# Kernel optimization log

Hardware: AMD Instinct MI355X
Metric: run time of the kernel (lower is better)

Reference implementation:

```python
import jax, jax.numpy as jnp
import numpy as np

B = 4096      # batch
D = 64        # state_dim
H = 512       # hidden_dim


def setup_inputs() -> dict:
    key = jax.random.key(0)
    ks = jax.random.split(key, 16)

    def init(k, shape, fan_in):
        return jax.random.normal(k, shape, dtype=jnp.float32) / np.float32(np.sqrt(fan_in))

    mu = jax.random.normal(ks[0], (B, D), dtype=jnp.float32)
    sigma_diag = 0.1 * jax.random.uniform(ks[1], (B, D), dtype=jnp.float32) + 0.01
    states = jnp.concatenate([mu, sigma_diag], axis=1)  # [B, 2D]

    return {
        "t": jnp.float32(0.5),
        "states": states,
        # dynamics net: tanh MLP D -> H -> H -> D
        "W1": init(ks[2], (H, D), D), "b1": jnp.zeros((H,), jnp.float32),
        "W2": init(ks[3], (H, H), H), "b2": jnp.zeros((H,), jnp.float32),
        "W3": init(ks[4], (D, H), H), "b3": jnp.zeros((D,), jnp.float32),
        # process-noise net: tanh MLP D -> H -> H -> D, softplus head (diagonal Q)
        "V1": init(ks[5], (H, D), D), "c1": jnp.zeros((H,), jnp.float32),
        "V2": init(ks[6], (H, H), H), "c2": jnp.zeros((H,), jnp.float32),
        "V3": init(ks[7], (D, H), H), "c3": jnp.zeros((D,), jnp.float32),
    }


def reference(t, states, W1, b1, W2, b2, W3, b3, V1, c1, V2, c2, V3, c3):
    # UPN ODE function, diagonal-covariance path.
    mu = states[:, :D]          # [B, D]
    sigma_diag = states[:, D:]  # [B, D]

    # dynamics MLP forward (t is an autonomous-system placeholder, unused)
    h1 = jnp.tanh(mu @ W1.T + b1)   # [B, H]
    h2 = jnp.tanh(h1 @ W2.T + b2)   # [B, H]
    mu_drift = h2 @ W3.T + b3       # [B, D]

    # analytic batched Jacobian of the tanh MLP: J = W3 diag(1-h2^2) W2 diag(1-h1^2) W1
    d1 = 1.0 - h1 * h1              # [B, H]
    d2 = 1.0 - h2 * h2              # [B, H]
    inner = jnp.einsum('hk,bk,kd->bhd', W2, d1, W1)   # [B, H, D]
    J = jnp.einsum('oh,bh,bhd->bod', W3, d2, inner)   # [B, D, D]
    J_diag = jnp.diagonal(J, axis1=1, axis2=2)        # [B, D]

    # process-noise net: diagonal Q, softplus ensures positivity
    g1 = jnp.tanh(mu @ V1.T + c1)
    g2 = jnp.tanh(g1 @ V2.T + c2)
    Q_diag = jax.nn.softplus(g2 @ V3.T + c3)          # [B, D]

    sigma_drift = 2.0 * J_diag * sigma_diag + Q_diag  # [B, D]
    return jnp.concatenate([mu_drift, sigma_drift], axis=1)  # [B, 2D]
```

## Files before the change

### kernel.cpp

```cpp
#include <hip/hip_runtime.h>
#include <hip/hip_bf16.h>

#define BB 4096
#define DD 64
#define HH 512

typedef __hip_bfloat16 bf16;
typedef _Float16 f16;
typedef __attribute__((ext_vector_type(8))) short bf16x8;
typedef __attribute__((ext_vector_type(8))) _Float16 f16x8;
typedef __attribute__((ext_vector_type(4))) float f32x4;

__device__ __forceinline__ float bf2f(bf16 x) { return __bfloat162float(x); }
__device__ __forceinline__ float u16tof(unsigned short u) {
  union { unsigned int i; float f; } v; v.i = ((unsigned int)u) << 16; return v.f;
}
#define BC8(p) __builtin_bit_cast(bf16x8, *(const uint4*)(p))
#define BCH8(p) __builtin_bit_cast(f16x8, *(const uint4*)(p))

__device__ __forceinline__ void gl16(const void* g, void* l) {
  __builtin_amdgcn_global_load_lds((__attribute__((address_space(1))) void*)g,
                                   (__attribute__((address_space(3))) void*)l,
                                   16, 0, 0);
}

#define BARRIER() __builtin_amdgcn_s_barrier()
#define LGKM0() do { asm volatile("s_waitcnt lgkmcnt(0)" ::: "memory"); \
                     __builtin_amdgcn_sched_barrier(0); } while (0)


__global__ __launch_bounds__(256) void cvt_weights(
    const float* __restrict__ W2, const float* __restrict__ V2,
    const float* __restrict__ W1, const float* __restrict__ V1,
    const float* __restrict__ W3, const float* __restrict__ V3,
    bf16* __restrict__ W2bf, bf16* __restrict__ V2bf,
    bf16* __restrict__ W1bf, bf16* __restrict__ V1bf,
    bf16* __restrict__ W3bf, bf16* __restrict__ V3bf,
    f16* __restrict__ W2sw, f16* __restrict__ W1sw, float* __restrict__ W3T) {
  int blk = blockIdx.x, t = threadIdx.x;
  if (blk < 512) {
    const float* src = (blk < 256) ? W2 : V2;
    bf16* dst = (blk < 256) ? W2bf : V2bf;
    int i = ((blk & 255) * 256 + t) * 4;
    float4 v = *(const float4*)(src + i);
    bf16 o[4] = {__float2bfloat16(v.x), __float2bfloat16(v.y),
                 __float2bfloat16(v.z), __float2bfloat16(v.w)};
    *(uint2*)(dst + i) = *(uint2*)o;
  } else if (blk < 640) {
    int uid = (blk - 512) * 256 + t;
    int kc = uid >> 12, rem = uid & 4095;
    int h = rem >> 3, u = rem & 7;
    const float* src = W2 + (size_t)h * HH + kc * 64 + u * 8;
    float4 a = *(const float4*)src;
    float4 b = *(const float4*)(src + 4);
    f16 o[8] = {(f16)a.x, (f16)a.y, (f16)a.z, (f16)a.w,
                (f16)b.x, (f16)b.y, (f16)b.z, (f16)b.w};
    *(uint4*)(W2sw + (size_t)((kc * 512 + h) * 8 + (u ^ (h & 7))) * 8) = *(uint4*)o;
  } else if (blk < 656) {
    int uid = (blk - 640) * 256 + t;
    int kc = uid >> 9, rem = uid & 511;
    int dl = rem >> 3, u = rem & 7;
    f16 o[8];
#pragma unroll
    for (int e = 0; e < 8; ++e)
      o[e] = (f16)W1[(size_t)(kc * 64 + u * 8 + e) * DD + dl];
    *(uint4*)(W1sw + (size_t)((kc * 64 + dl) * 8 + (u ^ (dl & 7))) * 8) = *(uint4*)o;
  } else if (blk < 784) {
    int which = (blk - 656) >> 5;
    int local = (blk - 656) & 31;
    const float* src = (which == 0) ? W1 : (which == 1) ? V1 : (which == 2) ? W3 : V3;
    bf16* dst = (which == 0) ? W1bf : (which == 1) ? V1bf : (which == 2) ? W3bf : V3bf;
    int i = (local * 256 + t) * 4;
    float4 v = *(const float4*)(src + i);
    bf16 o[4] = {__float2bfloat16(v.x), __float2bfloat16(v.y),
                 __float2bfloat16(v.z), __float2bfloat16(v.w)};
    *(uint2*)(dst + i) = *(uint2*)o;
  } else {
    int e = ((blk - 784) * 256 + t) * 4;
    int h = e >> 6, o0 = e & 63;
    float o[4];
#pragma unroll
    for (int j = 0; j < 4; ++j) o[j] = W3[(size_t)(o0 + j) * HH + h];
    *(float4*)(W3T + (size_t)h * 64 + o0) = *(float4*)o;
  }
}

__global__ __launch_bounds__(256) void fwd(
    const float* __restrict__ states,
    const bf16* __restrict__ W1bf, const float* __restrict__ b1,
    const bf16* __restrict__ W2bf, const float* __restrict__ b2,
    const bf16* __restrict__ W3bf, const float* __restrict__ b3,
    const bf16* __restrict__ V1bf, const float* __restrict__ c1,
    const bf16* __restrict__ V2bf, const float* __restrict__ c2,
    const bf16* __restrict__ V3bf, const float* __restrict__ c3,
    bf16* __restrict__ Xbf, bf16* __restrict__ Ybf, float* __restrict__ out) {
  __shared__ __align__(16) bf16 mus[16 * 72];
  __shared__ __align__(16) bf16 Xres[16 * 520];
  __shared__ __align__(16) bf16 Bs[128 * 72];
  __shared__ __align__(16) bf16 Ych[16 * 136];
  const int bt = blockIdx.x * 16;
  const int path = blockIdx.y;
  const bf16* Wa = path ? V1bf : W1bf;
  const float* ba = path ? c1 : b1;
  const bf16* Wb = path ? V2bf : W2bf;
  const float* bbv = path ? c2 : b2;
  const bf16* Wc = path ? V3bf : W3bf;
  const float* bcv = path ? c3 : b3;
  const int t = threadIdx.x;
  const int lane = t & 63;
  const int w = t >> 6;
  const int c = lane & 15, q = lane >> 4;

  if (t < 128) {
    int row = t >> 3, cg = (t & 7) * 8;
    bf16 o[8];
#pragma unroll
    for (int j = 0; j < 8; j += 4) {
      float4 v = *(const float4*)(states + (size_t)(bt + row) * 128 + cg + j);
      o[j] = __float2bfloat16(v.x); o[j + 1] = __float2bfloat16(v.y);
      o[j + 2] = __float2bfloat16(v.z); o[j + 3] = __float2bfloat16(v.w);
    }
    *(uint4*)(mus + row * 72 + cg) = *(const uint4*)o;
  }
  __syncthreads();

  for (int nch = 0; nch < 4; ++nch) {
    if (nch) __syncthreads();
#pragma unroll
    for (int i = 0; i < 4; ++i) {
      int g = t + i * 256;
      int row = g >> 3, kb = (g & 7) * 8;
      *(uint4*)(Bs + row * 72 + kb) =
          *(const uint4*)(Wa + (size_t)(nch * 128 + row) * 64 + kb);
    }
    __syncthreads();
    f32x4 acc1[2] = {};
#pragma unroll
    for (int s = 0; s < 2; ++s) {
      bf16x8 af = BC8(mus + c * 72 + s * 32 + q * 8);
#pragma unroll
      for (int nt = 0; nt < 2; ++nt) {
        bf16x8 bfr = BC8(Bs + (w * 32 + nt * 16 + c) * 72 + s * 32 + q * 8);
        acc1[nt] = __builtin_amdgcn_mfma_f32_16x16x32_bf16(af, bfr, acc1[nt], 0, 0, 0);
      }
    }
#pragma unroll
    for (int nt = 0; nt < 2; ++nt) {
      int col = nch * 128 + w * 32 + nt * 16 + c;
      float bias = ba[col];
#pragma unroll
      for (int r = 0; r < 4; ++r) {
        int row = q * 4 + r;
        float x = tanhf(acc1[nt][r] + bias);
        Xres[row * 520 + col] = __float2bfloat16(x);
        if (!path) Xbf[(size_t)(bt + row) * HH + col] = __float2bfloat16(x);
      }
    }
  }
  __syncthreads();

  f32x4 acc3 = {};
  for (int hch = 0; hch < 4; ++hch) {
    f32x4 acc2[2] = {};
    for (int kc = 0; kc < 8; ++kc) {
      __syncthreads();
#pragma unroll
      for (int i = 0; i < 4; ++i) {
        int g = t + i * 256;
        int row = g >> 3, kb = (g & 7) * 8;
        *(uint4*)(Bs + row * 72 + kb) =
            *(const uint4*)(Wb + (size_t)(hch * 128 + row) * HH + kc * 64 + kb);
      }
      __syncthreads();
#pragma unroll
      for (int s = 0; s < 2; ++s) {
        bf16x8 af = BC8(Xres + c * 520 + kc * 64 + s * 32 + q * 8);
#pragma unroll
        for (int nt = 0; nt < 2; ++nt) {
          bf16x8 bfr = BC8(Bs + (w * 32 + nt * 16 + c) * 72 + s * 32 + q * 8);
          acc2[nt] = __builtin_amdgcn_mfma_f32_16x16x32_bf16(af, bfr, acc2[nt], 0, 0, 0);
        }
      }
    }
    __syncthreads();
#pragma unroll
    for (int nt = 0; nt < 2; ++nt) {
      int hl = w * 32 + nt * 16 + c;
      int h = hch * 128 + hl;
      float bias = bbv[h];
#pragma unroll
      for (int r = 0; r < 4; ++r) {
        int row = q * 4 + r;
        float y = tanhf(acc2[nt][r] + bias);
        Ych[row * 136 + hl] = __float2bfloat16(y);
        if (!path) Ybf[(size_t)(bt + row) * HH + h] = __float2bfloat16(y);
      }
    }
    __syncthreads();
#pragma unroll
    for (int s3 = 0; s3 < 4; ++s3) {
      bf16x8 bf3 = BC8(Wc + (size_t)(w * 16 + c) * HH + hch * 128 + s3 * 32 + q * 8);
      bf16x8 af3 = BC8(Ych + c * 136 + s3 * 32 + q * 8);
      acc3 = __builtin_amdgcn_mfma_f32_16x16x32_bf16(af3, bf3, acc3, 0, 0, 0);
    }
  }
  {
    int o = w * 16 + c;
    float bias = bcv[o];
#pragma unroll
    for (int r = 0; r < 4; ++r) {
      int row = q * 4 + r;
      float v = acc3[r] + bias;
      if (path) {
        v = fmaxf(v, 0.0f) + log1pf(expf(-fabsf(v)));
        out[(size_t)(bt + row) * 128 + 64 + o] = v;
      } else {
        out[(size_t)(bt + row) * 128 + o] = v;
      }
    }
  }
}

#define LDSB(buf) ((buf) * 32768)
#define LDSA(buf) (98304 + (buf) * 8192)
#define LDSD1 122880
#define LDSD2 126976
#define LDSRED 98304

#define STAGE(kc_, buf_) do {                                                  \
    const char* gb_ = (const char*)W2sw + ((size_t)(kc_) * 512 + h0) * 128;    \
    char* lb_ = (char*)lds + LDSB(buf_);                                       \
    gl16(gb_ + t * 16, lb_ + t * 16);                                          \
    gl16(gb_ + 8192 + t * 16, lb_ + 8192 + t * 16);                            \
    gl16(gb_ + 16384 + t * 16, lb_ + 16384 + t * 16);                          \
    gl16(gb_ + 24576 + t * 16, lb_ + 24576 + t * 16);                          \
    gl16((const char*)W1sw + (kc_) * 8192 + t * 16,                            \
         (char*)lds + LDSA(buf_) + t * 16);                                    \
  } while (0)

__global__ __launch_bounds__(512, 2) void k4_gemm(
    const bf16* __restrict__ Xbf, const bf16* __restrict__ Ybf,
    const f16* __restrict__ W1sw, const f16* __restrict__ W2sw,
    const float* __restrict__ W3T, float* __restrict__ Jpart) {
  __shared__ __align__(16) char lds[131072];
  const int bt = blockIdx.x;
  const int h0 = blockIdx.y * 256;
  const int t = threadIdx.x;
  const int lane = t & 63;
  const int w = t >> 6;
  const int c = lane & 15, q = lane >> 4;
  const int wr = w >> 2, wc = w & 3;
  const int b0 = bt * 4;

  {
    int e = t * 4, j = e >> 9, k = e & 511;
    ushort4 xv = *(const ushort4*)((const unsigned short*)Xbf +
                                   (size_t)(b0 + j) * HH + k);
    f16 o[4];
    float x;
    x = u16tof(xv.x); o[0] = (f16)(1.f - x * x);
    x = u16tof(xv.y); o[1] = (f16)(1.f - x * x);
    x = u16tof(xv.z); o[2] = (f16)(1.f - x * x);
    x = u16tof(xv.w); o[3] = (f16)(1.f - x * x);
    *(uint2*)(lds + LDSD1 + e * 2) = *(uint2*)o;
  }
  {
    int e = t * 2, j = e >> 8, n = e & 255;
    ushort2 yv = *(const ushort2*)((const unsigned short*)Ybf +
                                   (size_t)(b0 + j) * HH + h0 + n);
    float y0 = u16tof(yv.x), y1 = u16tof(yv.y);
    float2 d2v = {1.f - y0 * y0, 1.f - y1 * y1};
    *(float2*)(lds + LDSD2 + e * 4) = d2v;
  }
  __syncthreads();

  STAGE(0, 0);
  STAGE(1, 1);
  asm volatile("s_waitcnt vmcnt(5)" ::: "memory");
  BARRIER();

  const int cj = c & 7;
  const int j16_0 = ((0 + q) ^ cj) * 16;
  const int j16_1 = ((4 + q) ^ cj) * 16;
  const int arow = c * 128;
  const int brow = (wc * 64 + c) * 128;
  const char* d1b = (const char*)lds + LDSD1 + wr * 2048 + q * 16;

  f32x4 acc[8][4] = {};

#pragma unroll
  for (int kc = 0; kc < 8; ++kc) {
    const char* Bb = (const char*)lds + LDSB(kc % 3);
    const char* Ab = (const char*)lds + LDSA(kc % 3);
    const char* gB2 = (const char*)W2sw + ((size_t)(kc + 2) * 512 + h0) * 128;
    const char* gA2 = (const char*)W1sw + (size_t)(kc + 2) * 8192;
    char* lB2 = (char*)lds + LDSB((kc + 2) % 3);
    char* lA2 = (char*)lds + LDSA((kc + 2) % 3);
    f16x8 av;

    f16x8 b0[4], a0[4];
    f16x8 d00 = BCH8(d1b + kc * 128);
#pragma unroll
    for (int nt = 0; nt < 4; ++nt) b0[nt] = BCH8(Bb + brow + nt * 2048 + j16_0);
#pragma unroll
    for (int i = 0; i < 4; ++i) a0[i] = BCH8(Ab + arow + i * 2048 + j16_0);
    if (kc < 6) {
      gl16(gB2 + t * 16, lB2 + t * 16);
      gl16(gB2 + 8192 + t * 16, lB2 + 8192 + t * 16);
    }
    BARRIER(); LGKM0();
    __builtin_amdgcn_s_setprio(1);
#pragma unroll
    for (int mt = 0; mt < 4; ++mt) {
      av = a0[mt] * d00;
#pragma unroll
      for (int nt = 0; nt < 4; ++nt)
        acc[mt][nt] = __builtin_amdgcn_mfma_f32_16x16x32_f16(
            av, b0[nt], acc[mt][nt], 0, 0, 0);
    }
    __builtin_amdgcn_s_setprio(0);
    BARRIER();

    f16x8 d10 = BCH8(d1b + 1024 + kc * 128);
    if (kc < 6) {
      gl16(gB2 + 16384 + t * 16, lB2 + 16384 + t * 16);
      gl16(gB2 + 24576 + t * 16, lB2 + 24576 + t * 16);
    }
    BARRIER(); LGKM0();
    __builtin_amdgcn_s_setprio(1);
#pragma unroll
    for (int mt = 0; mt < 4; ++mt) {
      av = a0[mt] * d10;
#pragma unroll
      for (int nt = 0; nt < 4; ++nt)
        acc[mt + 4][nt] = __builtin_amdgcn_mfma_f32_16x16x32_f16(
            av, b0[nt], acc[mt + 4][nt], 0, 0, 0);
    }
    __builtin_amdgcn_s_setprio(0);
    BARRIER();

    f16x8 b1[4], a1[4];
    f16x8 d01 = BCH8(d1b + 64 + kc * 128);
#pragma unroll
    for (int nt = 0; nt < 4; ++nt) b1[nt] = BCH8(Bb + brow + nt * 2048 + j16_1);
#pragma unroll
    for (int i = 0; i < 4; ++i) a1[i] = BCH8(Ab + arow + i * 2048 + j16_1);
    if (kc < 6) gl16(gA2 + t * 16, lA2 + t * 16);
    BARRIER(); LGKM0();
    __builtin_amdgcn_s_setprio(1);
#pragma unroll
    for (int mt = 0; mt < 4; ++mt) {
      av = a1[mt] * d01;
#pragma unroll
      for (int nt = 0; nt < 4; ++nt)
        acc[mt][nt] = __builtin_amdgcn_mfma_f32_16x16x32_f16(
            av, b1[nt], acc[mt][nt], 0, 0, 0);
    }
    __builtin_amdgcn_s_setprio(0);
    BARRIER();

    f16x8 d11 = BCH8(d1b + 1024 + 64 + kc * 128);
    BARRIER(); LGKM0();
    __builtin_amdgcn_s_setprio(1);
#pragma unroll
    for (int mt = 0; mt < 4; ++mt) {
      av = a1[mt] * d11;
#pragma unroll
      for (int nt = 0; nt < 4; ++nt)
        acc[mt + 4][nt] = __builtin_amdgcn_mfma_f32_16x16x32_f16(
            av, b1[nt], acc[mt + 4][nt], 0, 0, 0);
    }
    __builtin_amdgcn_s_setprio(0);
    if (kc < 6) {
      asm volatile("s_waitcnt vmcnt(5)" ::: "memory");
      BARRIER();
    } else if (kc == 6) {
      asm volatile("s_waitcnt vmcnt(0)" ::: "memory");
      BARRIER();
    }
  }
  __syncthreads();

#pragma unroll
  for (int i = 0; i < 8; ++i) {
    int e = (t + i * 512) * 4;
    int col = e >> 6, dl0 = e & 63;
    float4 v = *(const float4*)(W3T + (size_t)(h0 + col) * 64 + dl0);
    *(float4*)(lds + (col * 72 + dl0) * 4) = v;
  }
  __syncthreads();

  float d2r[2][4];
#pragma unroll
  for (int bh = 0; bh < 2; ++bh)
#pragma unroll
    for (int nt = 0; nt < 4; ++nt)
      d2r[bh][nt] = *(const float*)(
          lds + LDSD2 + ((wr * 2 + bh) * 256 + wc * 64 + nt * 16 + c) * 4);

  float vsum[8][4] = {};
#pragma unroll
  for (int mt4 = 0; mt4 < 4; ++mt4)
#pragma unroll
    for (int nt = 0; nt < 4; ++nt) {
      f32x4 w3v = *(const f32x4*)(
          lds + ((wc * 64 + nt * 16 + c) * 72 + mt4 * 16 + q * 4) * 4);
#pragma unroll
      for (int bh = 0; bh < 2; ++bh) {
        const int mt = bh * 4 + mt4;
        float sc = d2r[bh][nt];
#pragma unroll
        for (int r = 0; r < 4; ++r)
          vsum[mt][r] += acc[mt][nt][r] * w3v[r] * sc;
      }
    }

#pragma unroll
  for (int mt = 0; mt < 8; ++mt)
#pragma unroll
    for (int r = 0; r < 4; ++r) {
      float v = vsum[mt][r];
      v += __shfl_xor(v, 1);
      v += __shfl_xor(v, 2);
      v += __shfl_xor(v, 4);
      v += __shfl_xor(v, 8);
      if (c == 0)
        *(float*)(lds + LDSRED +
                  (wc * 256 + wr * 128 + mt * 16 + q * 4 + r) * 4) = v;
    }
  __syncthreads();
  if (t < 256) {
    float J = *(const float*)(lds + LDSRED + t * 4) +
              *(const float*)(lds + LDSRED + (256 + t) * 4) +
              *(const float*)(lds + LDSRED + (512 + t) * 4) +
              *(const float*)(lds + LDSRED + (768 + t) * 4);
    Jpart[(size_t)blockIdx.y * (BB * 64) + (size_t)bt * 256 + t] = J;
  }
}

__global__ __launch_bounds__(256) void combine(
    const float* __restrict__ Jpart, const float* __restrict__ states,
    float* __restrict__ out) {
  int idx = blockIdx.x * 256 + threadIdx.x;
  int b = idx >> 6, d = idx & 63;
  const int plane = BB * 64;
  float J = Jpart[idx] + Jpart[plane + idx];
  float sig = states[(size_t)b * 128 + 64 + d];
  float qd = out[(size_t)b * 128 + 64 + d];
  out[(size_t)b * 128 + 64 + d] = 2.0f * J * sig + qd;
}

extern "C" void kernel_launch(void* const* d_in, const int* in_sizes, int n_in,
                              void* d_out, int out_size, void* d_ws, size_t ws_size,
                              hipStream_t stream) {
  const float* states = (const float*)d_in[1];
  const float* W1 = (const float*)d_in[2];
  const float* b1 = (const float*)d_in[3];
  const float* W2 = (const float*)d_in[4];
  const float* b2 = (const float*)d_in[5];
  const float* W3 = (const float*)d_in[6];
  const float* b3 = (const float*)d_in[7];
  const float* V1 = (const float*)d_in[8];
  const float* c1 = (const float*)d_in[9];
  const float* V2 = (const float*)d_in[10];
  const float* c2 = (const float*)d_in[11];
  const float* V3 = (const float*)d_in[12];
  const float* c3 = (const float*)d_in[13];
  float* out = (float*)d_out;

  bf16* Xbf = (bf16*)d_ws;
  bf16* Ybf = Xbf + (size_t)BB * HH;
  bf16* W2bf = Ybf + (size_t)BB * HH;
  bf16* V2bf = W2bf + (size_t)HH * HH;
  bf16* W1bf = V2bf + (size_t)HH * HH;
  bf16* V1bf = W1bf + (size_t)HH * DD;
  bf16* W3bf = V1bf + (size_t)HH * DD;
  bf16* V3bf = W3bf + (size_t)DD * HH;
  f16* W1sw = (f16*)(V3bf + (size_t)DD * HH);
  f16* W2sw = W1sw + (size_t)DD * HH;
  float* W3T = (float*)(W2sw + (size_t)HH * HH);
  float* Jpart = W3T + (size_t)HH * DD;

  cvt_weights<<<dim3(816), 256, 0, stream>>>(W2, V2, W1, V1, W3, V3,
                                             W2bf, V2bf, W1bf, V1bf,
                                             W3bf, V3bf, W2sw, W1sw, W3T);
  fwd<<<dim3(256, 2), 256, 0, stream>>>(states, W1bf, b1, W2bf, b2, W3bf, b3,
                                        V1bf, c1, V2bf, c2, V3bf, c3,
                                        Xbf, Ybf, out);
  k4_gemm<<<dim3(1024, 2), 512, 0, stream>>>(Xbf, Ybf, W1sw, W2sw, W3T, Jpart);
  combine<<<dim3(1024), 256, 0, stream>>>(Jpart, states, out);
}
```

Measured before the change: 281.7 us.

## Software-pipeline LDS fragment loads ahead of MFMA clusters in Jacobian GEMM loop

Restructures the inner K loop so the A/B fragment and d1 loads for the next sub-step come from LDS while the current MFMA cluster runs, replacing the load-then-wait-lgkmcnt(0) pattern. It removes the explicit lgkmcnt waits and sched_barriers, cuts the barriers per iteration from eight to four, and moves the vmcnt wait to mid-iteration. The change adds register pressure from double-buffered fragments and relies on the compiler inserting correct LDS waits around the inline-asm barriers, which could risk races on the triple-buffered LDS.

```diff
diff --git a/kernel.cpp b/kernel.cpp
--- a/kernel.cpp
+++ b/kernel.cpp
@@ -24,9 +24,7 @@
                                    16, 0, 0);
 }
 
-#define BARRIER() __builtin_amdgcn_s_barrier()
-#define LGKM0() do { asm volatile("s_waitcnt lgkmcnt(0)" ::: "memory"); \
-                     __builtin_amdgcn_sched_barrier(0); } while (0)
+#define BARX() asm volatile("s_barrier" ::: "memory")
 
 
 __global__ __launch_bounds__(256) void cvt_weights(
@@ -277,7 +275,7 @@
   STAGE(0, 0);
   STAGE(1, 1);
   asm volatile("s_waitcnt vmcnt(5)" ::: "memory");
-  BARRIER();
+  BARX();
 
   const int cj = c & 7;
   const int j16_0 = ((0 + q) ^ cj) * 16;
@@ -286,98 +284,101 @@
   const int brow = (wc * 64 + c) * 128;
   const char* d1b = (const char*)lds + LDSD1 + wr * 2048 + q * 16;
 
+  f16x8 aS0[4], bS0[4], aS1[4], bS1[4], d00, d10, d01, d11, av;
+#pragma unroll
+  for (int i = 0; i < 4; ++i) aS0[i] = BCH8(lds + LDSA(0) + arow + i * 2048 + j16_0);
+#pragma unroll
+  for (int nt = 0; nt < 4; ++nt) bS0[nt] = BCH8(lds + LDSB(0) + brow + nt * 2048 + j16_0);
+  d00 = BCH8(d1b + 0 * 128);
+  d10 = BCH8(d1b + 1024 + 0 * 128);
+
   f32x4 acc[8][4] = {};
 
 #pragma unroll
   for (int kc = 0; kc < 8; ++kc) {
     const char* Bb = (const char*)lds + LDSB(kc % 3);
     const char* Ab = (const char*)lds + LDSA(kc % 3);
+    const char* Bn = (const char*)lds + LDSB((kc + 1) % 3);
+    const char* An = (const char*)lds + LDSA((kc + 1) % 3);
     const char* gB2 = (const char*)W2sw + ((size_t)(kc + 2) * 512 + h0) * 128;
     const char* gA2 = (const char*)W1sw + (size_t)(kc + 2) * 8192;
     char* lB2 = (char*)lds + LDSB((kc + 2) % 3);
     char* lA2 = (char*)lds + LDSA((kc + 2) % 3);
-    f16x8 av;
-
-    f16x8 b0[4], a0[4];
-    f16x8 d00 = BCH8(d1b + kc * 128);
-#pragma unroll
-    for (int nt = 0; nt < 4; ++nt) b0[nt] = BCH8(Bb + brow + nt * 2048 + j16_0);
-#pragma unroll
-    for (int i = 0; i < 4; ++i) a0[i] = BCH8(Ab + arow + i * 2048 + j16_0);
+
+#pragma unroll
+    for (int i = 0; i < 4; ++i) aS1[i] = BCH8(Ab + arow + i * 2048 + j16_1);
+    d01 = BCH8(d1b + 64 + kc * 128);
     if (kc < 6) {
       gl16(gB2 + t * 16, lB2 + t * 16);
       gl16(gB2 + 8192 + t * 16, lB2 + 8192 + t * 16);
     }
-    BARRIER(); LGKM0();
     __builtin_amdgcn_s_setprio(1);
 #pragma unroll
     for (int mt = 0; mt < 4; ++mt) {
-      av = a0[mt] * d00;
+      av = aS0[mt] * d00;
 #pragma unroll
       for (int nt = 0; nt < 4; ++nt)
         acc[mt][nt] = __builtin_amdgcn_mfma_f32_16x16x32_f16(
-            av, b0[nt], acc[mt][nt], 0, 0, 0);
+            av, bS0[nt], acc[mt][nt], 0, 0, 0);
     }
     __builtin_amdgcn_s_setprio(0);
-    BARRIER();
-
-    f16x8 d10 = BCH8(d1b + 1024 + kc * 128);
+    BARX();
+
+#pragma unroll
+    for (int nt = 0; nt < 4; ++nt) bS1[nt] = BCH8(Bb + brow + nt * 2048 + j16_1);
+    d11 = BCH8(d1b + 1024 + 64 + kc * 128);
     if (kc < 6) {
       gl16(gB2 + 16384 + t * 16, lB2 + 16384 + t * 16);
       gl16(gB2 + 24576 + t * 16, lB2 + 24576 + t * 16);
     }
-    BARRIER(); LGKM0();
     __builtin_amdgcn_s_setprio(1);
 #pragma unroll
     for (int mt = 0; mt < 4; ++mt) {
-      av = a0[mt] * d10;
+      av = aS0[mt] * d10;
 #pragma unroll
       for (int nt = 0; nt < 4; ++nt)
         acc[mt + 4][nt] = __builtin_amdgcn_mfma_f32_16x16x32_f16(
-            av, b0[nt], acc[mt + 4][nt], 0, 0, 0);
+            av, bS0[nt], acc[mt + 4][nt], 0, 0, 0);
     }
     __builtin_amdgcn_s_setprio(0);
-    BARRIER();
-
-    f16x8 b1[4], a1[4];
-    f16x8 d01 = BCH8(d1b + 64 + kc * 128);
-#pragma unroll
-    for (int nt = 0; nt < 4; ++nt) b1[nt] = BCH8(Bb + brow + nt * 2048 + j16_1);
-#pragma unroll
-    for (int i = 0; i < 4; ++i) a1[i] = BCH8(Ab + arow + i * 2048 + j16_1);
+    if (kc < 6)      asm volatile("s_waitcnt vmcnt(4)" ::: "memory");
+    else if (kc == 6) asm volatile("s_waitcnt vmcnt(0)" ::: "memory");
+    BARX();
+
+    if (kc < 7) {
+#pragma unroll
+      for (int i = 0; i < 4; ++i) aS0[i] = BCH8(An + arow + i * 2048 + j16_0);
+      d00 = BCH8(d1b + (kc + 1) * 128);
+    }
     if (kc < 6) gl16(gA2 + t * 16, lA2 + t * 16);
-    BARRIER(); LGKM0();
     __builtin_amdgcn_s_setprio(1);
 #pragma unroll
     for (int mt = 0; mt < 4; ++mt) {
-      av = a1[mt] * d01;
+      av = aS1[mt] * d01;
 #pragma unroll
       for (int nt = 0; nt < 4; ++nt)
         acc[mt][nt] = __builtin_amdgcn_mfma_f32_16x16x32_f16(
-            av, b1[nt], acc[mt][nt], 0, 0, 0);
+            av, bS1[nt], acc[mt][nt], 0, 0, 0);
     }
     __builtin_amdgcn_s_setprio(0);
-    BARRIER();
-
-    f16x8 d11 = BCH8(d1b + 1024 + 64 + kc * 128);
-    BARRIER(); LGKM0();
+    BARX();
+
+    if (kc < 7) {
+#pragma unroll
+      for (int nt = 0; nt < 4; ++nt) bS0[nt] = BCH8(Bn + brow + nt * 2048 + j16_0);
+      d10 = BCH8(d1b + 1024 + (kc + 1) * 128);
+    }
     __builtin_amdgcn_s_setprio(1);
 #pragma unroll
     for (int mt = 0; mt < 4; ++mt) {
-      av = a1[mt] * d11;
+      av = aS1[mt] * d11;
 #pragma unroll
       for (int nt = 0; nt < 4; ++nt)
         acc[mt + 4][nt] = __builtin_amdgcn_mfma_f32_16x16x32_f16(
-            av, b1[nt], acc[mt + 4][nt], 0, 0, 0);
+            av, bS1[nt], acc[mt + 4][nt], 0, 0, 0);
     }
     __builtin_amdgcn_s_setprio(0);
-    if (kc < 6) {
-      asm volatile("s_waitcnt vmcnt(5)" ::: "memory");
-      BARRIER();
-    } else if (kc == 6) {
-      asm volatile("s_waitcnt vmcnt(0)" ::: "memory");
-      BARRIER();
-    }
+    BARX();
   }
   __syncthreads();
 
```

New measurement: 278.0 us. Within noise of the previous version (-1.3%).

## Load W2 B-fragments directly from global into registers, drop LDS staging

Applied to the files above, without the earlier changes.

The W2 operand is pre-arranged by the conversion kernel into a fragment-ordered layout, so each wave can load its MFMA B fragments straight from global memory into registers, double-buffered one k-chunk ahead. W1 is now loaded whole into LDS once at kernel start, and the per-chunk barriers, LDS triple-buffering and waitcnt choreography are removed. This cuts LDS traffic and synchronisation and shrinks the LDS footprint. The cost is that MFMA now depends on global/L2 load latency, with only one chunk of lookahead to hide it, and the fragment registers raise register pressure.

```diff
diff --git a/kernel.cpp b/kernel.cpp
--- a/kernel.cpp
+++ b/kernel.cpp
@@ -23,10 +23,6 @@
                                    (__attribute__((address_space(3))) void*)l,
                                    16, 0, 0);
 }
-
-#define BARRIER() __builtin_amdgcn_s_barrier()
-#define LGKM0() do { asm volatile("s_waitcnt lgkmcnt(0)" ::: "memory"); \
-                     __builtin_amdgcn_sched_barrier(0); } while (0)
 
 
 __global__ __launch_bounds__(256) void cvt_weights(
@@ -36,7 +32,7 @@
     bf16* __restrict__ W2bf, bf16* __restrict__ V2bf,
     bf16* __restrict__ W1bf, bf16* __restrict__ V1bf,
     bf16* __restrict__ W3bf, bf16* __restrict__ V3bf,
-    f16* __restrict__ W2sw, f16* __restrict__ W1sw, float* __restrict__ W3T) {
+    f16* __restrict__ W2fr, f16* __restrict__ W1sw, float* __restrict__ W3T) {
   int blk = blockIdx.x, t = threadIdx.x;
   if (blk < 512) {
     const float* src = (blk < 256) ? W2 : V2;
@@ -48,14 +44,15 @@
     *(uint2*)(dst + i) = *(uint2*)o;
   } else if (blk < 640) {
     int uid = (blk - 512) * 256 + t;
-    int kc = uid >> 12, rem = uid & 4095;
-    int h = rem >> 3, u = rem & 7;
-    const float* src = W2 + (size_t)h * HH + kc * 64 + u * 8;
+    int col = (uid >> 2) & 511;
+    int kc2s = uid >> 11;
+    int kc = kc2s >> 1, s = kc2s & 1, q = uid & 3;
+    const float* src = W2 + (size_t)col * HH + kc * 64 + s * 32 + q * 8;
     float4 a = *(const float4*)src;
     float4 b = *(const float4*)(src + 4);
     f16 o[8] = {(f16)a.x, (f16)a.y, (f16)a.z, (f16)a.w,
                 (f16)b.x, (f16)b.y, (f16)b.z, (f16)b.w};
-    *(uint4*)(W2sw + (size_t)((kc * 512 + h) * 8 + (u ^ (h & 7))) * 8) = *(uint4*)o;
+    *(uint4*)(W2fr + (size_t)uid * 8) = *(uint4*)o;
   } else if (blk < 656) {
     int uid = (blk - 640) * 256 + t;
     int kc = uid >> 9, rem = uid & 511;
@@ -221,28 +218,16 @@
   }
 }
 
-#define LDSB(buf) ((buf) * 32768)
-#define LDSA(buf) (98304 + (buf) * 8192)
-#define LDSD1 122880
-#define LDSD2 126976
-#define LDSRED 98304
-
-#define STAGE(kc_, buf_) do {                                                  \
-    const char* gb_ = (const char*)W2sw + ((size_t)(kc_) * 512 + h0) * 128;    \
-    char* lb_ = (char*)lds + LDSB(buf_);                                       \
-    gl16(gb_ + t * 16, lb_ + t * 16);                                          \
-    gl16(gb_ + 8192 + t * 16, lb_ + 8192 + t * 16);                            \
-    gl16(gb_ + 16384 + t * 16, lb_ + 16384 + t * 16);                          \
-    gl16(gb_ + 24576 + t * 16, lb_ + 24576 + t * 16);                          \
-    gl16((const char*)W1sw + (kc_) * 8192 + t * 16,                            \
-         (char*)lds + LDSA(buf_) + t * 16);                                    \
-  } while (0)
+#define LDSW1 0
+#define LDSD1 65536
+#define LDSD2 73728
+#define LDSRED 77824
 
 __global__ __launch_bounds__(512, 2) void k4_gemm(
     const bf16* __restrict__ Xbf, const bf16* __restrict__ Ybf,
-    const f16* __restrict__ W1sw, const f16* __restrict__ W2sw,
+    const f16* __restrict__ W1sw, const f16* __restrict__ W2fr,
     const float* __restrict__ W3T, float* __restrict__ Jpart) {
-  __shared__ __align__(16) char lds[131072];
+  __shared__ __align__(16) char lds[81920];
   const int bt = blockIdx.x;
   const int h0 = blockIdx.y * 256;
   const int t = threadIdx.x;
@@ -252,6 +237,10 @@
   const int wr = w >> 2, wc = w & 3;
   const int b0 = bt * 4;
 
+#pragma unroll
+  for (int i = 0; i < 8; ++i)
+    gl16((const char*)W1sw + (t + i * 512) * 16,
+         (char*)lds + LDSW1 + (t + i * 512) * 16);
   {
     int e = t * 4, j = e >> 9, k = e & 511;
     ushort4 xv = *(const ushort4*)((const unsigned short*)Xbf +
@@ -274,41 +263,46 @@
   }
   __syncthreads();
 
-  STAGE(0, 0);
-  STAGE(1, 1);
-  asm volatile("s_waitcnt vmcnt(5)" ::: "memory");
-  BARRIER();
-
   const int cj = c & 7;
   const int j16_0 = ((0 + q) ^ cj) * 16;
   const int j16_1 = ((4 + q) ^ cj) * 16;
   const int arow = c * 128;
-  const int brow = (wc * 64 + c) * 128;
   const char* d1b = (const char*)lds + LDSD1 + wr * 2048 + q * 16;
 
+  const char* gB = (const char*)W2fr + (size_t)(h0 + wc * 64) * 64 +
+                   (c * 64 + q * 16);
+#define BLD(kc_, s_, nt_) \
+  BCH8(gB + ((kc_) * 2 + (s_)) * 32768 + (nt_) * 1024)
+
+  f16x8 bb0[2][4], bb1[2][4];
+#pragma unroll
+  for (int nt = 0; nt < 4; ++nt) bb0[0][nt] = BLD(0, 0, nt);
+#pragma unroll
+  for (int nt = 0; nt < 4; ++nt) bb1[0][nt] = BLD(0, 1, nt);
+
   f32x4 acc[8][4] = {};
 
 #pragma unroll
   for (int kc = 0; kc < 8; ++kc) {
-    const char* Bb = (const char*)lds + LDSB(kc % 3);
-    const char* Ab = (const char*)lds + LDSA(kc % 3);
-    const char* gB2 = (const char*)W2sw + ((size_t)(kc + 2) * 512 + h0) * 128;
-    const char* gA2 = (const char*)W1sw + (size_t)(kc + 2) * 8192;
-    char* lB2 = (char*)lds + LDSB((kc + 2) % 3);
-    char* lA2 = (char*)lds + LDSA((kc + 2) % 3);
+    const int cur = kc & 1, nxt = cur ^ 1;
+    if (kc < 7) {
+#pragma unroll
+      for (int nt = 0; nt < 4; ++nt) bb0[nxt][nt] = BLD(kc + 1, 0, nt);
+#pragma unroll
+      for (int nt = 0; nt < 4; ++nt) bb1[nxt][nt] = BLD(kc + 1, 1, nt);
+    }
+    const char* Ab = (const char*)lds + LDSW1 + kc * 8192;
+    f16x8 a0[4], a1[4];
+#pragma unroll
+    for (int i = 0; i < 4; ++i) a0[i] = BCH8(Ab + arow + i * 2048 + j16_0);
+#pragma unroll
+    for (int i = 0; i < 4; ++i) a1[i] = BCH8(Ab + arow + i * 2048 + j16_1);
+    f16x8 d00 = BCH8(d1b + kc * 128);
+    f16x8 d10 = BCH8(d1b + 1024 + kc * 128);
+    f16x8 d01 = BCH8(d1b + 64 + kc * 128);
+    f16x8 d11 = BCH8(d1b + 1024 + 64 + kc * 128);
+
     f16x8 av;
-
-    f16x8 b0[4], a0[4];
-    f16x8 d00 = BCH8(d1b + kc * 128);
-#pragma unroll
-    for (int nt = 0; nt < 4; ++nt) b0[nt] = BCH8(Bb + brow + nt * 2048 + j16_0);
-#pragma unroll
-    for (int i = 0; i < 4; ++i) a0[i] = BCH8(Ab + arow + i * 2048 + j16_0);
-    if (kc < 6) {
-      gl16(gB2 + t * 16, lB2 + t * 16);
-      gl16(gB2 + 8192 + t * 16, lB2 + 8192 + t * 16);
-    }
-    BARRIER(); LGKM0();
     __builtin_amdgcn_s_setprio(1);
 #pragma unroll
     for (int mt = 0; mt < 4; ++mt) {
@@ -316,68 +310,34 @@
 #pragma unroll
       for (int nt = 0; nt < 4; ++nt)
         acc[mt][nt] = __builtin_amdgcn_mfma_f32_16x16x32_f16(
-            av, b0[nt], acc[mt][nt], 0, 0, 0);
-    }
-    __builtin_amdgcn_s_setprio(0);
-    BARRIER();
-
-    f16x8 d10 = BCH8(d1b + 1024 + kc * 128);
-    if (kc < 6) {
-      gl16(gB2 + 16384 + t * 16, lB2 + 16384 + t * 16);
-      gl16(gB2 + 24576 + t * 16, lB2 + 24576 + t * 16);
-    }
-    BARRIER(); LGKM0();
-    __builtin_amdgcn_s_setprio(1);
+            av, bb0[cur][nt], acc[mt][nt], 0, 0, 0);
+    }
 #pragma unroll
     for (int mt = 0; mt < 4; ++mt) {
       av = a0[mt] * d10;
 #pragma unroll
       for (int nt = 0; nt < 4; ++nt)
         acc[mt + 4][nt] = __builtin_amdgcn_mfma_f32_16x16x32_f16(
-            av, b0[nt], acc[mt + 4][nt], 0, 0, 0);
-    }
-    __builtin_amdgcn_s_setprio(0);
-    BARRIER();
-
-    f16x8 b1[4], a1[4];
-    f16x8 d01 = BCH8(d1b + 64 + kc * 128);
-#pragma unroll
-    for (int nt = 0; nt < 4; ++nt) b1[nt] = BCH8(Bb + brow + nt * 2048 + j16_1);
-#pragma unroll
-    for (int i = 0; i < 4; ++i) a1[i] = BCH8(Ab + arow + i * 2048 + j16_1);
-    if (kc < 6) gl16(gA2 + t * 16, lA2 + t * 16);
-    BARRIER(); LGKM0();
-    __builtin_amdgcn_s_setprio(1);
+            av, bb0[cur][nt], acc[mt + 4][nt], 0, 0, 0);
+    }
 #pragma unroll
     for (int mt = 0; mt < 4; ++mt) {
       av = a1[mt] * d01;
 #pragma unroll
       for (int nt = 0; nt < 4; ++nt)
         acc[mt][nt] = __builtin_amdgcn_mfma_f32_16x16x32_f16(
-            av, b1[nt], acc[mt][nt], 0, 0, 0);
-    }
-    __builtin_amdgcn_s_setprio(0);
-    BARRIER();
-
-    f16x8 d11 = BCH8(d1b + 1024 + 64 + kc * 128);
-    BARRIER(); LGKM0();
-    __builtin_amdgcn_s_setprio(1);
+            av, bb1[cur][nt], acc[mt][nt], 0, 0, 0);
+    }
 #pragma unroll
     for (int mt = 0; mt < 4; ++mt) {
       av = a1[mt] * d11;
 #pragma unroll
       for (int nt = 0; nt < 4; ++nt)
         acc[mt + 4][nt] = __builtin_amdgcn_mfma_f32_16x16x32_f16(
-            av, b1[nt], acc[mt + 4][nt], 0, 0, 0);
+            av, bb1[cur][nt], acc[mt + 4][nt], 0, 0, 0);
     }
     __builtin_amdgcn_s_setprio(0);
-    if (kc < 6) {
-      asm volatile("s_waitcnt vmcnt(5)" ::: "memory");
-      BARRIER();
-    } else if (kc == 6) {
-      asm volatile("s_waitcnt vmcnt(0)" ::: "memory");
-      BARRIER();
-    }
+    __builtin_amdgcn_sched_barrier(0);
   }
   __syncthreads();
 
@@ -477,16 +437,16 @@
   bf16* W3bf = V1bf + (size_t)HH * DD;
   bf16* V3bf = W3bf + (size_t)DD * HH;
   f16* W1sw = (f16*)(V3bf + (size_t)DD * HH);
-  f16* W2sw = W1sw + (size_t)DD * HH;
-  float* W3T = (float*)(W2sw + (size_t)HH * HH);
+  f16* W2fr = W1sw + (size_t)DD * HH;
+  float* W3T = (float*)(W2fr + (size_t)HH * HH);
   float* Jpart = W3T + (size_t)HH * DD;
 
   cvt_weights<<<dim3(816), 256, 0, stream>>>(W2, V2, W1, V1, W3, V3,
                                              W2bf, V2bf, W1bf, V1bf,
-                                             W3bf, V3bf, W2sw, W1sw, W3T);
+                                             W3bf, V3bf, W2fr, W1sw, W3T);
   fwd<<<dim3(256, 2), 256, 0, stream>>>(states, W1bf, b1, W2bf, b2, W3bf, b3,
                                         V1bf, c1, V2bf, c2, V3bf, c3,
                                         Xbf, Ybf, out);
-  k4_gemm<<<dim3(1024, 2), 512, 0, stream>>>(Xbf, Ybf, W1sw, W2sw, W3T, Jpart);
+  k4_gemm<<<dim3(1024, 2), 512, 0, stream>>>(Xbf, Ybf, W1sw, W2fr, W3T, Jpart);
   combine<<<dim3(1024), 256, 0, stream>>>(Jpart, states, out);
 }
```

Measured after the change: 269.2 us. 1.05x faster.
